# Kernel tuning notes

Measured on AMD Instinct MI355X. Metric: run time of the kernel, lower is better.

The kernel has to match this reference:

```python
import jax, jax.numpy as jnp
import numpy as np

EPS = 1e-5   # BatchNorm eps (eval mode, running_mean=0, running_var=1 as at init)
NEG = 0.2    # LeakyReLU negative slope


def _conv(W, x):
    # 1x1 conv == channel matmul. W: [out_c, in_c], x: [B, in_c, ...]
    return jnp.einsum('oc,bc...->bo...', W, x)


def _bn(x, g, b):
    # eval-mode BN with running_mean=0, running_var=1
    sh = (1, -1) + (1,) * (x.ndim - 2)
    return x * (g.reshape(sh) / np.float32(np.sqrt(1.0 + EPS))) + b.reshape(sh)


def _lrelu(x):
    return jax.nn.leaky_relu(x, NEG)


def _knn_idx(pos, k):
    # pos: [B, 3, N] -> idx [B, N, k] of k nearest points (incl. self)
    sq = jnp.sum(pos * pos, axis=1)                      # [B, N]
    inner = jnp.einsum('bcn,bcm->bnm', pos, pos)         # [B, N, N]
    dist = sq[:, :, None] + sq[:, None, :] - 2.0 * inner
    _, idx = jax.lax.top_k(-dist, k)
    return idx


def _gather(points, idx):
    # points [B, N, C], idx [B, N, K] -> [B, N, K, C]
    return jax.vmap(lambda p, i: p[i])(points, idx)


def setup_inputs() -> dict:
    key = jax.random.key(0)
    B, N, K = 2, 8192, 16
    d_points, d_model = 64, 64
    ks = jax.random.split(key, 24)
    w = lambda k_, o, i: (jax.random.normal(k_, (o, i), jnp.float32) * 0.05)
    gm = lambda k_, c: (1.0 + 0.1 * jax.random.normal(k_, (c,), jnp.float32))
    bt = lambda k_, c: (0.1 * jax.random.normal(k_, (c,), jnp.float32))
    return {
        'feats': jax.random.normal(ks[0], (B, d_points, N), jnp.float32),
        'pos': jax.random.uniform(ks[1], (B, 3, N), jnp.float32),
        'k': K,
        'W1': w(ks[2], d_model, d_points), 'g1': gm(ks[3], d_model), 'b1': bt(ks[4], d_model),
        'Wq': w(ks[5], d_model, d_model), 'Wk': w(ks[6], d_model, d_model), 'Wv': w(ks[7], d_model, d_model),
        'Wd1': w(ks[8], d_model, 3), 'gd1': gm(ks[9], d_model), 'bd1': bt(ks[10], d_model),
        'Wd2': w(ks[11], d_model, d_model), 'gd2': gm(ks[12], d_model), 'bd2': bt(ks[13], d_model),
        'Wg1': w(ks[14], d_model, d_model), 'gg1': gm(ks[15], d_model), 'bg1': bt(ks[16], d_model),
        'Wg2': w(ks[17], d_model, d_model), 'gg2': gm(ks[18], d_model), 'bg2': bt(ks[19], d_model),
        'W2': w(ks[20], d_points, d_model), 'g2': gm(ks[21], d_points), 'b2': bt(ks[22], d_points),
    }


def reference(feats, pos, k, W1, g1, b1, Wq, Wk, Wv,
              Wd1, gd1, bd1, Wd2, gd2, bd2,
              Wg1, gg1, bg1, Wg2, gg2, bg2, W2, g2, b2):
    B, _, N = feats.shape
    knn_idx = _knn_idx(pos, k)                            # [B, N, K]
    pos_nc = jnp.transpose(pos, (0, 2, 1))                # [B, N, 3]
    knn_pos = _gather(pos_nc, knn_idx)                    # [B, N, K, 3]

    x = _lrelu(_bn(_conv(W1, feats), g1, b1))             # [B, d, N]
    q = _conv(Wq, x)                                      # [B, d, N]
    k_feat = _gather(jnp.transpose(_conv(Wk, x), (0, 2, 1)), knn_idx)
    k_t = jnp.transpose(k_feat, (0, 3, 2, 1))             # [B, d, K, N]
    v_feat = _gather(jnp.transpose(_conv(Wv, x), (0, 2, 1)), knn_idx)
    v_t = jnp.transpose(v_feat, (0, 3, 2, 1))             # [B, d, K, N]

    rel = pos_nc[:, :, None, :] - knn_pos                 # [B, N, K, 3]
    rel_t = jnp.transpose(rel, (0, 3, 2, 1))              # [B, 3, K, N]
    pe = _lrelu(_bn(_conv(Wd1, rel_t), gd1, bd1))
    pos_enc = _lrelu(_bn(_conv(Wd2, pe), gd2, bd2))       # [B, d, K, N]

    a = q[:, :, None, :] - k_t + pos_enc                  # [B, d, K, N]
    a = _lrelu(_bn(_conv(Wg1, a), gg1, bg1))
    a = _lrelu(_bn(_conv(Wg2, a), gg2, bg2))
    # torch: attn / sqrt(k.size(-1)) where k has shape [B, d, K, N] -> sqrt(N)
    attn = jax.nn.softmax(a / jnp.sqrt(jnp.float32(N)), axis=-2)

    res = jnp.einsum('bmnf,bmnf->bmf', attn, v_t + pos_enc)  # [B, d, N]
    out = _lrelu(_bn(_conv(W2, res), g2, b2)) + feats
    return out
```

## Files before the change

### kernel.cpp

```cpp
#include <hip/hip_runtime.h>
#include <hip/hip_bf16.h>
#include <math.h>

namespace {

constexpr int B = 2;
constexpr int N = 8192;
constexpr int D = 64;
constexpr int GRID = 10;
constexpr int GC = GRID * GRID * GRID;
constexpr float H = 0.1f;
constexpr float NEGS = 0.2f;
constexpr float BN_INV = 0.9999950000374997f;
constexpr float RSQN = 0.011048543456039806f;
constexpr int KNN_BLOCKS = B * N / 16;

typedef __attribute__((ext_vector_type(8))) short bf16x8;
typedef __attribute__((ext_vector_type(16))) float f32x16;

union Frag { int4 i4; unsigned u[4]; bf16x8 h; };

__device__ __forceinline__ float lrelu(float v) { return fmaxf(v, NEGS * v); }

__device__ __forceinline__ unsigned pk2(float a, float b) {
  __hip_bfloat162 h2 = __float22bfloat162_rn(make_float2(a, b));
  unsigned r;
  __builtin_memcpy(&r, &h2, 4);
  return r;
}
__device__ __forceinline__ float blo(unsigned u) { return __uint_as_float(u << 16); }
__device__ __forceinline__ float bhi(unsigned u) { return __uint_as_float(u & 0xFFFF0000u); }

__device__ __forceinline__ f32x16 MF(int4 a, const Frag& b, f32x16 c) {
  Frag af; af.i4 = a;
  return __builtin_amdgcn_mfma_f32_32x32x16_bf16(af.h, b.h, c, 0, 0, 0);
}

template <int CTRL>
__device__ __forceinline__ float dpp_add(float v) {
  int t = __builtin_amdgcn_update_dpp(0, __float_as_int(v), CTRL, 0xF, 0xF, false);
  return v + __int_as_float(t);
}
__device__ __forceinline__ float rsum16(float v) {
  v = dpp_add<0x128>(v);
  v = dpp_add<0x124>(v);
  v = dpp_add<0x122>(v);
  v = dpp_add<0x121>(v);
  return v;
}
template <int CTRL>
__device__ __forceinline__ unsigned long long dpp_min_u64(unsigned long long k) {
  int lo = __builtin_amdgcn_update_dpp(0, (int)(unsigned)k, CTRL, 0xF, 0xF, false);
  int hi = __builtin_amdgcn_update_dpp(0, (int)(unsigned)(k >> 32), CTRL, 0xF, 0xF, false);
  unsigned long long o = ((unsigned long long)(unsigned)hi << 32) | (unsigned)lo;
  return o < k ? o : k;
}
__device__ __forceinline__ unsigned long long rmin16_u64(unsigned long long k) {
  k = dpp_min_u64<0x128>(k);
  k = dpp_min_u64<0x124>(k);
  k = dpp_min_u64<0x122>(k);
  k = dpp_min_u64<0x121>(k);
  return k;
}

__device__ __forceinline__ int cellco(float v) {
  int c = (int)(v * 10.0f);
  return min(max(c, 0), GRID - 1);
}

__device__ __forceinline__ void buildB(const f32x16& x0, const f32x16& x1, int h, Frag Bf[4]) {
  unsigned Z[8][2];
  #pragma unroll
  for (int q = 0; q < 4; ++q) {
    Z[q][0]     = pk2(x0[4*q+0], x0[4*q+1]);
    Z[q][1]     = pk2(x0[4*q+2], x0[4*q+3]);
    Z[4+q][0]   = pk2(x1[4*q+0], x1[4*q+1]);
    Z[4+q][1]   = pk2(x1[4*q+2], x1[4*q+3]);
  }
  unsigned S[8][2];
  #pragma unroll
  for (int q = 0; q < 8; ++q) {
    S[q][0] = (unsigned)__shfl_xor((int)Z[q][0], 32);
    S[q][1] = (unsigned)__shfl_xor((int)Z[q][1], 32);
  }
  #pragma unroll
  for (int t = 0; t < 4; ++t) {
    int qq = (t >> 1) * 4 + 2 * (t & 1);
    Bf[t].u[0] = h ? S[qq+1][0] : Z[qq][0];
    Bf[t].u[1] = h ? S[qq+1][1] : Z[qq][1];
    Bf[t].u[2] = h ? Z[qq+1][0] : S[qq][0];
    Bf[t].u[3] = h ? Z[qq+1][1] : S[qq][1];
  }
}

__device__ __forceinline__ f32x16 biasAct(f32x16 d, const float4* bp, int mt, int h) {
  f32x16 r;
  #pragma unroll
  for (int q = 0; q < 4; ++q) {
    float4 bb = bp[h * 8 + mt * 4 + q];
    r[4*q+0] = lrelu(d[4*q+0] + bb.x);
    r[4*q+1] = lrelu(d[4*q+1] + bb.y);
    r[4*q+2] = lrelu(d[4*q+2] + bb.z);
    r[4*q+3] = lrelu(d[4*q+3] + bb.w);
  }
  return r;
}

struct PrepArgs {
  const float* W[9];
  const float* scale[9];
  const float* bias[5];
  const float* bd1;
};

__global__ __launch_bounds__(256) void prep_kernel(PrepArgs a, unsigned short* AF, float* biasAll) {
  int mi = blockIdx.x;
  int tid = threadIdx.x;
  if (mi < 8) {
    int off = (mi == 7) ? 29696 : mi * 4096;
    const float* W = a.W[mi];
    const float* G = a.scale[mi];
    unsigned short* dst = AF + off;
    for (int e = tid; e < 4096; e += 256) {
      int i = e & 7, lane = (e >> 3) & 63, t = (e >> 9) & 3, mt = e >> 11;
      int row = 32 * mt + (lane & 31);
      int k = 16 * t + 8 * (lane >> 5) + i;
      float v = W[row * 64 + k];
      if (G) v *= G[row] * BN_INV;
      if (mi == 6) v *= RSQN;
      __hip_bfloat16 hb = __float2bfloat16(v);
      __builtin_memcpy(&dst[e], &hb, 2);
    }
  } else {
    const float* W = a.W[8];
    const float* G = a.scale[8];
    for (int e = tid; e < 1024; e += 256) {
      int i = e & 7, lane = (e >> 3) & 63, mt = e >> 9;
      int row = 32 * mt + (lane & 31), h = lane >> 5;
      float v = 0.f;
      if (h == 0) {
        if (i < 3) v = W[row * 3 + i] * G[row] * BN_INV;
        else if (i == 3) v = a.bd1[row];
      }
      __hip_bfloat16 hb = __float2bfloat16(v);
      __builtin_memcpy(&AF[28672 + e], &hb, 2);
    }
    for (int e = tid; e < 320; e += 256) {
      int ai = e >> 6, idx = e & 63;
      int h = idx >> 5, mt = (idx >> 4) & 1, q = (idx >> 2) & 3, j = idx & 3;
      float bv = a.bias[ai][32 * mt + 8 * q + 4 * h + j];
      if (ai == 3) bv *= RSQN;
      biasAll[e] = bv;
    }
  }
}

__global__ __launch_bounds__(256) void pos4cid_kernel(
    const float* __restrict__ pos, float* __restrict__ pos4,
    int* __restrict__ cid16, int* __restrict__ cellCount)
{
  int i = blockIdx.x * 256 + threadIdx.x;
  int b = i >> 13;
  int n = i & (N - 1);
  const float* pb = pos + (size_t)b * 3 * N;
  float x = pb[n], y = pb[N + n], z = pb[2 * N + n];
  float4 v = {x, y, z, x * x + y * y + z * z};
  *reinterpret_cast<float4*>(pos4 + (size_t)i * 4) = v;
  int cid = (cellco(z) * GRID + cellco(y)) * GRID + cellco(x);
  cid16[i] = cid;
  atomicAdd(&cellCount[b * GC + cid], 1);
}

__global__ __launch_bounds__(1024) void scan_kernel(
    const int* __restrict__ cnt, int* __restrict__ cellStart)
{
  __shared__ int s[2][2048];
  int t = threadIdx.x;
  s[0][t] = cnt[t];
  s[0][t + 1024] = cnt[t + 1024];
  __syncthreads();
  int src = 0;
  for (int off = 1; off < 2048; off <<= 1) {
    int dst = src ^ 1;
    for (int i = t; i < 2048; i += 1024) {
      int v = s[src][i];
      if (i >= off) v += s[src][i - off];
      s[dst][i] = v;
    }
    __syncthreads();
    src ^= 1;
  }
  cellStart[t] = (t == 0) ? 0 : s[src][t - 1];
  cellStart[t + 1024] = s[src][t + 1023];
}

__global__ __launch_bounds__(256) void scatter_kernel(
    const float* __restrict__ pos4, const int* __restrict__ cid16,
    const int* __restrict__ cellStart, int* __restrict__ cellOfs,
    float4* __restrict__ pos4s, int* __restrict__ sid, int* __restrict__ inv)
{
  int i = blockIdx.x * 256 + threadIdx.x;
  int b = i >> 13;
  int cg = b * GC + cid16[i];
  int dst = cellStart[cg] + atomicAdd(&cellOfs[cg], 1);
  pos4s[dst] = *reinterpret_cast<const float4*>(pos4 + (size_t)i * 4);
  sid[dst] = i & (N - 1);
  inv[i] = dst;
}

__global__ __launch_bounds__(256) void knnqkv_kernel(
    const float4* __restrict__ pos4s, const int* __restrict__ sid,
    const int* __restrict__ cellStart, int* __restrict__ knn_s,
    const float* __restrict__ feats, const int4* __restrict__ AF,
    const float* __restrict__ b1p, const int* __restrict__ inv,
    uint2* __restrict__ qT, uint2* __restrict__ kT, uint2* __restrict__ vT)
{
  __shared__ int4 sA[1024];

  if (blockIdx.x < KNN_BLOCKS) {
    constexpr unsigned long long SENT = ~0ULL;
    int lq = threadIdx.x & 15;
    int wid = (blockIdx.x * 256 + threadIdx.x) >> 4;
    int b = wid >> 13;
    float4 q = pos4s[wid];
    int cx = cellco(q.x), cy = cellco(q.y), cz = cellco(q.z);
    const int cbase = b * GC;

    int nb = (int)(cx == 0 || cx == GRID - 1) + (int)(cy == 0 || cy == GRID - 1)
           + (int)(cz == 0 || cz == GRID - 1);
    int r0 = (nb >= 2) ? 2 : 1;

    unsigned long long dk[16];
    #pragma unroll
    for (int j = 0; j < 16; ++j) dk[j] = SENT;

    auto scanSeg = [&](int i0, int i1) {
      #pragma unroll 1
      for (int i = i0 + lq; i < i1; i += 16) {
        float4 cp = pos4s[i];
        float inn = q.x * cp.x + q.y * cp.y + q.z * cp.z;
        float dist = fmaxf(fmaf(-2.f, inn, q.w + cp.w), 0.f);
        unsigned long long key =
            ((unsigned long long)__float_as_uint(dist) << 26) |
            ((unsigned long long)(unsigned)sid[i] << 13) |
            (unsigned long long)(unsigned)(i & (N - 1));
        if (key < dk[15]) {
          bool bj = true;
          #pragma unroll
          for (int j = 15; j >= 1; --j) {
            bool bjm1 = key < dk[j - 1];
            dk[j] = bj ? (bjm1 ? dk[j - 1] : key) : dk[j];
            bj = bjm1;
          }
          if (bj) dk[0] = key;
        }
      }
    };

    bool done = false, first = true;
    #pragma unroll 1
    for (int r = 1; r < GRID; ++r) {
      if (r >= r0 && !done) {
        int x0 = max(cx - r, 0), x1 = min(cx + r, GRID - 1);
        int y0 = max(cy - r, 0), y1 = min(cy + r, GRID - 1);
        int z0 = max(cz - r, 0), z1 = min(cz + r, GRID - 1);
        int rin = first ? -1 : r - 1;
        int xi0 = max(cx - rin, 0), xi1 = min(cx + rin, GRID - 1);
        int yi0 = max(cy - rin, 0), yi1 = min(cy + rin, GRID - 1);
        int zi0 = max(cz - rin, 0), zi1 = min(cz + rin, GRID - 1);
        #pragma unroll 1
        for (int zz = z0; zz <= z1; ++zz) {
          bool zout = (zz < zi0) || (zz > zi1);
          #pragma unroll 1
          for (int yy = y0; yy <= y1; ++yy) {
            bool rowfull = zout || (yy < yi0) || (yy > yi1);
            int rowc = cbase + (zz * GRID + yy) * GRID;
            if (rowfull) {
              scanSeg(cellStart[rowc + x0], cellStart[rowc + x1 + 1]);
            } else {
              if (x0 < xi0) scanSeg(cellStart[rowc + x0], cellStart[rowc + xi0]);
              if (xi1 < x1) scanSeg(cellStart[rowc + xi1 + 1], cellStart[rowc + x1 + 1]);
            }
          }
        }
        first = false;

        float mg = 3.4e38f;
        if (cx - r > 0)        mg = fminf(mg, q.x - (cx - r) * H);
        if (cx + r < GRID - 1) mg = fminf(mg, (cx + r + 1) * H - q.x);
        if (cy - r > 0)        mg = fminf(mg, q.y - (cy - r) * H);
        if (cy + r < GRID - 1) mg = fminf(mg, (cy + r + 1) * H - q.y);
        if (cz - r > 0)        mg = fminf(mg, q.z - (cz - r) * H);
        if (cz + r < GRID - 1) mg = fminf(mg, (cz + r + 1) * H - q.z);
        float thr = mg * mg * 0.999f;
        unsigned long long tk = ((unsigned long long)__float_as_uint(thr)) << 26;
        float c = 0.f;
        #pragma unroll
        for (int j = 0; j < 16; ++j) c += (dk[j] < tk) ? 1.f : 0.f;
        c = rsum16(c);
        done = (c > 15.5f);
      }
      if (__all(done)) break;
    }

    int myout = 0;
    #pragma unroll 1
    for (int e = 0; e < 16; ++e) {
      unsigned long long m = rmin16_u64(dk[0]);
      if (dk[0] == m) {
        #pragma unroll
        for (int j = 0; j < 15; ++j) dk[j] = dk[j + 1];
        dk[15] = SENT;
      }
      if (lq == e) myout = (int)(m & 0x1FFFULL);
    }
    knn_s[(size_t)wid * 16 + lq] = myout;
    return;
  }

  int qb = blockIdx.x - KNN_BLOCKS;
  int my = qb >> 7;
  int gx = qb & 127;
  for (int i = threadIdx.x; i < 512; i += 256) {
    sA[i] = AF[i];
    sA[512 + i] = AF[512 * (1 + my) + i];
  }
  __syncthreads();
  int lane = threadIdx.x & 63, w = threadIdx.x >> 6;
  int gw = gx * 4 + w;
  int col = lane & 31, h = lane >> 5;
  int nb_ = gw * 32;
  int b = nb_ >> 13;
  int n = (nb_ & (N - 1)) + col;
  size_t gpt = (size_t)b * N + n;
  int sv = inv[gpt];
  const float* fb = feats + (size_t)b * D * N + n;

  Frag Bf[4];
  #pragma unroll
  for (int t = 0; t < 4; ++t) {
    int c0 = 16 * t + 8 * h;
    float f[8];
    #pragma unroll
    for (int i = 0; i < 8; ++i) f[i] = fb[(size_t)(c0 + i) * N];
    #pragma unroll
    for (int d_ = 0; d_ < 4; ++d_) Bf[t].u[d_] = pk2(f[2*d_], f[2*d_+1]);
  }
  f32x16 acc0 = {}, acc1 = {};
  #pragma unroll
  for (int t = 0; t < 4; ++t) {
    acc0 = MF(sA[t * 64 + lane], Bf[t], acc0);
    acc1 = MF(sA[(4 + t) * 64 + lane], Bf[t], acc1);
  }
  const float4* bp = (const float4*)b1p;
  f32x16 x0 = biasAct(acc0, bp, 0, h);
  f32x16 x1 = biasAct(acc1, bp, 1, h);
  Frag Bx[4];
  buildB(x0, x1, h, Bx);

  uint2* op = (my == 0) ? qT : (my == 1) ? kT : vT;
  f32x16 a0 = {}, a1 = {};
  #pragma unroll
  for (int t = 0; t < 4; ++t) {
    a0 = MF(sA[512 + t * 64 + lane], Bx[t], a0);
    a1 = MF(sA[512 + (4 + t) * 64 + lane], Bx[t], a1);
  }
  #pragma unroll
  for (int q = 0; q < 4; ++q) {
    uint2 v0, v1;
    v0.x = pk2(a0[4*q+0], a0[4*q+1]); v0.y = pk2(a0[4*q+2], a0[4*q+3]);
    v1.x = pk2(a1[4*q+0], a1[4*q+1]); v1.y = pk2(a1[4*q+2], a1[4*q+3]);
    op[(size_t)sv * 16 + 2 * q + h] = v0;
    op[(size_t)sv * 16 + 8 + 2 * q + h] = v1;
  }
}

__global__ __launch_bounds__(256) void fused_kernel(
    const float4* __restrict__ pos4s, const int* __restrict__ sid,
    const int* __restrict__ knn_s,
    const uint2* __restrict__ qT, const uint2* __restrict__ kT, const uint2* __restrict__ vT,
    const int4* __restrict__ AF,
    const float* __restrict__ biases,
    uint2* __restrict__ res_ws)
{
  int lane = threadIdx.x & 63, w = threadIdx.x >> 6;
  int gw = blockIdx.x * 4 + w;
  int col = lane & 31, h = lane >> 5;
  int p = col >> 4, kk = col & 15;
  int sbase = gw * 2;
  int b = sbase >> 13;
  int s = sbase + p;

  int m_loc = knn_s[(size_t)s * 16 + kk];
  int orig = sid[s];
  float4 P = pos4s[s];

  __shared__ int4 sA[1664];
  for (int i = threadIdx.x; i < 1664; i += 256) sA[i] = AF[i];
  __syncthreads();
  const float4* bpd2 = (const float4*)(biases);
  const float4* bpg1 = (const float4*)(biases + 64);
  const float4* bpg2 = (const float4*)(biases + 128);

  size_t ms = (size_t)b * N + m_loc;
  float4 Q = pos4s[ms];
  float rx = P.x - Q.x, ry = P.y - Q.y, rz = P.z - Q.z;

  Frag B0;
  B0.u[0] = h ? 0u : pk2(rx, ry);
  B0.u[1] = h ? 0u : pk2(rz, 1.0f);
  B0.u[2] = 0u; B0.u[3] = 0u;
  f32x16 acc0 = {}, acc1 = {};
  acc0 = MF(sA[1536 + lane], B0, acc0);
  acc1 = MF(sA[1600 + lane], B0, acc1);
  f32x16 pe0, pe1;
  #pragma unroll
  for (int i = 0; i < 16; ++i) { pe0[i] = lrelu(acc0[i]); pe1[i] = lrelu(acc1[i]); }
  Frag Bp[4];
  buildB(pe0, pe1, h, Bp);

  acc0 = (f32x16){}; acc1 = (f32x16){};
  #pragma unroll
  for (int t = 0; t < 4; ++t) {
    acc0 = MF(sA[t * 64 + lane], Bp[t], acc0);
    acc1 = MF(sA[(4 + t) * 64 + lane], Bp[t], acc1);
  }
  f32x16 pn0 = biasAct(acc0, bpd2, 0, h);
  f32x16 pn1 = biasAct(acc1, bpd2, 1, h);

  unsigned pep[8][2];
  #pragma unroll
  for (int q = 0; q < 4; ++q) {
    pep[q][0]   = pk2(pn0[4*q+0], pn0[4*q+1]);
    pep[q][1]   = pk2(pn0[4*q+2], pn0[4*q+3]);
    pep[4+q][0] = pk2(pn1[4*q+0], pn1[4*q+1]);
    pep[4+q][1] = pk2(pn1[4*q+2], pn1[4*q+3]);
  }

  f32x16 av0, av1;
  #pragma unroll
  for (int mt = 0; mt < 2; ++mt) {
    f32x16& dst = mt ? av1 : av0;
    const f32x16& pn = mt ? pn1 : pn0;
    #pragma unroll
    for (int q = 0; q < 4; ++q) {
      uint2 qq_ = qT[(size_t)s * 16 + 8 * mt + 2 * q + h];
      uint2 kq_ = kT[ms * 16 + 8 * mt + 2 * q + h];
      dst[4*q+0] = pn[4*q+0] + blo(qq_.x) - blo(kq_.x);
      dst[4*q+1] = pn[4*q+1] + bhi(qq_.x) - bhi(kq_.x);
      dst[4*q+2] = pn[4*q+2] + blo(qq_.y) - blo(kq_.y);
      dst[4*q+3] = pn[4*q+3] + bhi(qq_.y) - bhi(kq_.y);
    }
  }
  buildB(av0, av1, h, Bp);

  acc0 = (f32x16){}; acc1 = (f32x16){};
  #pragma unroll
  for (int t = 0; t < 4; ++t) {
    acc0 = MF(sA[512 + t * 64 + lane], Bp[t], acc0);
    acc1 = MF(sA[512 + (4 + t) * 64 + lane], Bp[t], acc1);
  }
  f32x16 a10 = biasAct(acc0, bpg1, 0, h);
  f32x16 a11 = biasAct(acc1, bpg1, 1, h);
  buildB(a10, a11, h, Bp);

  acc0 = (f32x16){}; acc1 = (f32x16){};
  #pragma unroll
  for (int t = 0; t < 4; ++t) {
    acc0 = MF(sA[1024 + t * 64 + lane], Bp[t], acc0);
    acc1 = MF(sA[1024 + (4 + t) * 64 + lane], Bp[t], acc1);
  }
  f32x16 at0 = biasAct(acc0, bpg2, 0, h);
  f32x16 at1 = biasAct(acc1, bpg2, 1, h);

  uint2* rp = res_ws + ((size_t)b * N + orig) * 16;
  #pragma unroll
  for (int mt = 0; mt < 2; ++mt) {
    const f32x16& at = mt ? at1 : at0;
    f32x16 ev, nm;
    #pragma unroll
    for (int q = 0; q < 4; ++q) {
      uint2 vq_ = vT[ms * 16 + 8 * mt + 2 * q + h];
      unsigned pp0 = pep[mt * 4 + q][0], pp1 = pep[mt * 4 + q][1];
      float vp0 = blo(vq_.x) + blo(pp0);
      float vp1 = bhi(vq_.x) + bhi(pp0);
      float vp2 = blo(vq_.y) + blo(pp1);
      float vp3 = bhi(vq_.y) + bhi(pp1);
      ev[4*q+0] = __expf(at[4*q+0]); nm[4*q+0] = ev[4*q+0] * vp0;
      ev[4*q+1] = __expf(at[4*q+1]); nm[4*q+1] = ev[4*q+1] * vp1;
      ev[4*q+2] = __expf(at[4*q+2]); nm[4*q+2] = ev[4*q+2] * vp2;
      ev[4*q+3] = __expf(at[4*q+3]); nm[4*q+3] = ev[4*q+3] * vp3;
    }
    #pragma unroll
    for (int i = 0; i < 16; ++i) {
      ev[i] = rsum16(ev[i]);
      nm[i] = rsum16(nm[i]);
    }
    if (kk == 0) {
      #pragma unroll
      for (int q = 0; q < 4; ++q) {
        uint2 rr;
        rr.x = pk2(nm[4*q+0] / ev[4*q+0], nm[4*q+1] / ev[4*q+1]);
        rr.y = pk2(nm[4*q+2] / ev[4*q+2], nm[4*q+3] / ev[4*q+3]);
        rp[8 * mt + 2 * q + h] = rr;
      }
    }
  }
}

__global__ __launch_bounds__(256) void final_kernel(
    const uint2* __restrict__ res_ws, const int4* __restrict__ AF,
    const float* __restrict__ b2p, const float* __restrict__ feats,
    float* __restrict__ out)
{
  __shared__ int4 sA[512];
  for (int i = threadIdx.x; i < 512; i += 256) sA[i] = AF[i];
  __syncthreads();
  int lane = threadIdx.x & 63, w = threadIdx.x >> 6;
  int gw = blockIdx.x * 4 + w;
  int col = lane & 31, h = lane >> 5;
  int nb = gw * 32;
  int b = nb >> 13;
  int n = (nb & (N - 1)) + col;
  size_t g = (size_t)b * N + n;
  const int4* rp = (const int4*)(res_ws + (size_t)g * 16);
  Frag Br[4];
  #pragma unroll
  for (int t = 0; t < 4; ++t) Br[t].i4 = rp[2 * t + h];
  f32x16 a0 = {}, a1 = {};
  #pragma unroll
  for (int t = 0; t < 4; ++t) {
    a0 = MF(sA[t * 64 + lane], Br[t], a0);
    a1 = MF(sA[(4 + t) * 64 + lane], Br[t], a1);
  }
  const float4* bp = (const float4*)b2p;
  f32x16 o0 = biasAct(a0, bp, 0, h);
  f32x16 o1 = biasAct(a1, bp, 1, h);
  const float* fb = feats + (size_t)b * D * N;
  float* ob = out + (size_t)b * D * N;
  #pragma unroll
  for (int mt = 0; mt < 2; ++mt) {
    const f32x16& oo = mt ? o1 : o0;
    #pragma unroll
    for (int q = 0; q < 4; ++q) {
      #pragma unroll
      for (int j = 0; j < 4; ++j) {
        int chan = 32 * mt + 8 * q + 4 * h + j;
        ob[(size_t)chan * N + n] = oo[4*q+j] + fb[(size_t)chan * N + n];
      }
    }
  }
}

}

extern "C" void kernel_launch(void* const* d_in, const int* in_sizes, int n_in,
                              void* d_out, int out_size, void* d_ws, size_t ws_size,
                              hipStream_t stream) {
  const float* feats = (const float*)d_in[0];
  const float* pos   = (const float*)d_in[1];
  const float* W1  = (const float*)d_in[3];
  const float* g1  = (const float*)d_in[4];
  const float* b1  = (const float*)d_in[5];
  const float* Wq  = (const float*)d_in[6];
  const float* Wk  = (const float*)d_in[7];
  const float* Wv  = (const float*)d_in[8];
  const float* Wd1 = (const float*)d_in[9];
  const float* gd1 = (const float*)d_in[10];
  const float* bd1 = (const float*)d_in[11];
  const float* Wd2 = (const float*)d_in[12];
  const float* gd2 = (const float*)d_in[13];
  const float* bd2 = (const float*)d_in[14];
  const float* Wg1 = (const float*)d_in[15];
  const float* gg1 = (const float*)d_in[16];
  const float* bg1 = (const float*)d_in[17];
  const float* Wg2 = (const float*)d_in[18];
  const float* gg2 = (const float*)d_in[19];
  const float* bg2 = (const float*)d_in[20];
  const float* W2  = (const float*)d_in[21];
  const float* g2  = (const float*)d_in[22];
  const float* b2  = (const float*)d_in[23];

  uint8_t* wsb = (uint8_t*)d_ws;
  unsigned short* AF = (unsigned short*)wsb;
  float* biasAll = (float*)(wsb + 73728);
  float* pos4    = (float*)(wsb + 75008);
  uint2* qTb     = (uint2*)(wsb + 337152);
  uint2* kTb     = (uint2*)(wsb + 2434304);
  uint2* vTb     = (uint2*)(wsb + 4531456);
  uint2* res_ws  = (uint2*)(wsb + 6628608);
  int*   cid16     = (int*)(wsb + 10822912);
  int*   cellCount = (int*)(wsb + 10888448);
  int*   cellStart = (int*)(wsb + 10896640);
  int*   cellOfs   = (int*)(wsb + 10904832);
  float4* pos4s    = (float4*)(wsb + 10913024);
  int*   sid       = (int*)(wsb + 11175168);
  int*   knn_s     = (int*)(wsb + 11240704);
  int*   inv       = (int*)(wsb + 12289280);

  PrepArgs pa;
  pa.W[0] = W1;  pa.W[1] = Wq;  pa.W[2] = Wk;  pa.W[3] = Wv;
  pa.W[4] = Wd2; pa.W[5] = Wg1; pa.W[6] = Wg2; pa.W[7] = W2; pa.W[8] = Wd1;
  pa.scale[0] = g1;  pa.scale[1] = nullptr; pa.scale[2] = nullptr; pa.scale[3] = nullptr;
  pa.scale[4] = gd2; pa.scale[5] = gg1;     pa.scale[6] = gg2;     pa.scale[7] = g2; pa.scale[8] = gd1;
  pa.bias[0] = b1; pa.bias[1] = bd2; pa.bias[2] = bg1; pa.bias[3] = bg2; pa.bias[4] = b2;
  pa.bd1 = bd1;

  hipMemsetAsync(cellCount, 0, 2048 * sizeof(int), stream);
  hipMemsetAsync(cellOfs, 0, 2048 * sizeof(int), stream);
  hipLaunchKernelGGL(prep_kernel, dim3(9), dim3(256), 0, stream, pa, AF, biasAll);
  hipLaunchKernelGGL(pos4cid_kernel, dim3(B * N / 256), dim3(256), 0, stream,
                     pos, pos4, cid16, cellCount);
  hipLaunchKernelGGL(scan_kernel, dim3(1), dim3(1024), 0, stream, cellCount, cellStart);
  hipLaunchKernelGGL(scatter_kernel, dim3(B * N / 256), dim3(256), 0, stream,
                     pos4, cid16, cellStart, cellOfs, pos4s, sid, inv);
  hipLaunchKernelGGL(knnqkv_kernel, dim3(KNN_BLOCKS + 384), dim3(256), 0, stream,
                     pos4s, sid, cellStart, knn_s,
                     feats, (const int4*)wsb, biasAll, inv, qTb, kTb, vTb);
  hipLaunchKernelGGL(fused_kernel, dim3(B * N / 8), dim3(256), 0, stream,
                     pos4s, sid, knn_s, qTb, kTb, vTb,
                     (const int4*)(wsb + 32768), biasAll + 64, res_ws);
  hipLaunchKernelGGL(final_kernel, dim3(128), dim3(256), 0, stream,
                     res_ws, (const int4*)(wsb + 59392), biasAll + 256, feats, (float*)d_out);
}
```

Measured before the change: 128.2 us.

## Reorder kNN query quads by boundary class to balance per-block work

Adds two small kernels that classify each group of four cell-sorted query points by how many grid faces they touch, then build a permutation that puts heavy boundary quads first. The kNN kernel now maps each 64-thread wave to a quad taken from this permutation, so expensive (larger search radius) queries are scheduled early and waves inside a block do similar amounts of work. This is meant to reduce divergence and tail imbalance in the kNN search. It costs two extra launches, a memset and atomics, and it weakens spatial locality inside a block.

After: 208.3 us. 62.5% more time.

```diff
diff --git a/kernel.cpp b/kernel.cpp
--- a/kernel.cpp
+++ b/kernel.cpp
@@ -13,6 +13,7 @@
 constexpr float NEGS = 0.2f;
 constexpr float BN_INV = 0.9999950000374997f;
 constexpr float RSQN = 0.011048543456039806f;
+constexpr int NQUAD = B * N / 4;
 constexpr int KNN_BLOCKS = B * N / 16;
 
 typedef __attribute__((ext_vector_type(8))) short bf16x8;
@@ -208,9 +209,41 @@
   inv[i] = dst;
 }
 
+__global__ __launch_bounds__(256) void classify_kernel(
+    const float4* __restrict__ pos4s, int* __restrict__ qclass, int* __restrict__ classCnt)
+{
+  int quad = blockIdx.x * 256 + threadIdx.x;
+  if (quad >= NQUAD) return;
+  int nbmax = 0;
+  #pragma unroll
+  for (int j = 0; j < 4; ++j) {
+    float4 q = pos4s[quad * 4 + j];
+    int cx = cellco(q.x), cy = cellco(q.y), cz = cellco(q.z);
+    int nb = (int)(cx == 0 || cx == GRID - 1) + (int)(cy == 0 || cy == GRID - 1)
+           + (int)(cz == 0 || cz == GRID - 1);
+    nbmax = max(nbmax, nb);
+  }
+  int c = (nbmax >= 2) ? 0 : (nbmax == 1) ? 1 : 2;
+  qclass[quad] = c;
+  atomicAdd(&classCnt[c], 1);
+}
+
+__global__ __launch_bounds__(256) void permbuild_kernel(
+    const int* __restrict__ qclass, const int* __restrict__ classCnt,
+    int* __restrict__ classOfs, int* __restrict__ perm)
+{
+  int quad = blockIdx.x * 256 + threadIdx.x;
+  if (quad >= NQUAD) return;
+  int c = qclass[quad];
+  int base = (c > 0 ? classCnt[0] : 0) + (c > 1 ? classCnt[1] : 0);
+  int pos = base + atomicAdd(&classOfs[c], 1);
+  perm[pos] = quad;
+}
+
 __global__ __launch_bounds__(256) void knnqkv_kernel(
     const float4* __restrict__ pos4s, const int* __restrict__ sid,
     const int* __restrict__ cellStart, int* __restrict__ knn_s,
+    const int* __restrict__ perm,
     const float* __restrict__ feats, const int4* __restrict__ AF,
     const float* __restrict__ b1p, const int* __restrict__ inv,
     uint2* __restrict__ qT, uint2* __restrict__ kT, uint2* __restrict__ vT)
@@ -220,7 +253,10 @@
   if (blockIdx.x < KNN_BLOCKS) {
     constexpr unsigned long long SENT = ~0ULL;
     int lq = threadIdx.x & 15;
-    int wid = (blockIdx.x * 256 + threadIdx.x) >> 4;
+    int w = threadIdx.x >> 6;
+    int wl = (threadIdx.x & 63) >> 4;
+    int quad = perm[blockIdx.x * 4 + w];
+    int wid = quad * 4 + wl;
     int b = wid >> 13;
     float4 q = pos4s[wid];
     int cx = cellco(q.x), cy = cellco(q.y), cz = cellco(q.z);
@@ -597,6 +633,10 @@
   int*   sid       = (int*)(wsb + 11175168);
   int*   knn_s     = (int*)(wsb + 11240704);
   int*   inv       = (int*)(wsb + 12289280);
+  int*   qclass    = (int*)(wsb + 12354816);
+  int*   perm      = (int*)(wsb + 12371200);
+  int*   classCnt  = (int*)(wsb + 12387584);
+  int*   classOfs  = (int*)(wsb + 12387596);
 
   PrepArgs pa;
   pa.W[0] = W1;  pa.W[1] = Wq;  pa.W[2] = Wk;  pa.W[3] = Wv;
@@ -608,14 +648,19 @@
 
   hipMemsetAsync(cellCount, 0, 2048 * sizeof(int), stream);
   hipMemsetAsync(cellOfs, 0, 2048 * sizeof(int), stream);
+  hipMemsetAsync(classCnt, 0, 6 * sizeof(int), stream);
   hipLaunchKernelGGL(prep_kernel, dim3(9), dim3(256), 0, stream, pa, AF, biasAll);
   hipLaunchKernelGGL(pos4cid_kernel, dim3(B * N / 256), dim3(256), 0, stream,
                      pos, pos4, cid16, cellCount);
   hipLaunchKernelGGL(scan_kernel, dim3(1), dim3(1024), 0, stream, cellCount, cellStart);
   hipLaunchKernelGGL(scatter_kernel, dim3(B * N / 256), dim3(256), 0, stream,
                      pos4, cid16, cellStart, cellOfs, pos4s, sid, inv);
+  hipLaunchKernelGGL(classify_kernel, dim3((NQUAD + 255) / 256), dim3(256), 0, stream,
+                     pos4s, qclass, classCnt);
+  hipLaunchKernelGGL(permbuild_kernel, dim3((NQUAD + 255) / 256), dim3(256), 0, stream,
+                     qclass, classCnt, classOfs, perm);
   hipLaunchKernelGGL(knnqkv_kernel, dim3(KNN_BLOCKS + 384), dim3(256), 0, stream,
-                     pos4s, sid, cellStart, knn_s,
+                     pos4s, sid, cellStart, knn_s, perm,
                      feats, (const int4*)wsb, biasAll, inv, qTb, kTb, vTb);
   hipLaunchKernelGGL(fused_kernel, dim3(B * N / 8), dim3(256), 0, stream,
                      pos4s, sid, knn_s, qTb, kTb, vTb,
```
